# Kernel tuning notes

Measured on AMD Instinct MI355X. Metric: run time of the kernel, lower is better.

## Reference

```python
import jax, jax.numpy as jnp
import numpy as np

NUM_EXPERTS = 8


def setup_inputs() -> dict:
    key = jax.random.key(0)
    k1, k2, k3, k4, k5 = jax.random.split(key, 5)
    T, D, DFF, E, K = 2048, 2048, 1024, NUM_EXPERTS, 2
    hidden_states = jax.random.normal(k1, (T, D), dtype=jnp.float32)
    w1 = jax.random.normal(k2, (E, 2 * DFF, D), dtype=jnp.float32) * 0.02
    w2 = jax.random.normal(k3, (E, D, DFF), dtype=jnp.float32) * 0.02
    topk_weights = jax.random.uniform(k4, (T, K), dtype=jnp.float32)
    topk_weights = topk_weights / jnp.sum(topk_weights, axis=-1, keepdims=True)
    topk_ids = jax.random.randint(k5, (T, K), 0, E, dtype=jnp.int32)
    return {"hidden_states": hidden_states, "w1": w1, "w2": w2,
            "topk_weights": topk_weights, "topk_ids": topk_ids}


def _expert_fn(x, w1_e, w2_e):
    # x: [T, D], w1_e: [2*DFF, D], w2_e: [D, DFF]
    gu = x @ w1_e.T                      # [T, 2*DFF]
    dff = w2_e.shape[1]
    gate, up = gu[:, :dff], gu[:, dff:]
    h = jax.nn.silu(gate) * up           # SiLU-and-mul activation
    return h @ w2_e.T                    # [T, D]


def reference(hidden_states, w1, w2, topk_weights, topk_ids):
    T = hidden_states.shape[0]
    E = w1.shape[0]
    # route[t, e] = sum_k topk_weights[t,k] * (topk_ids[t,k] == e)
    route = jnp.zeros((T, E), dtype=hidden_states.dtype)
    route = route.at[jnp.arange(T)[:, None], topk_ids].add(topk_weights)
    # per-expert dense GEMMs (E is small and fixed), then weighted combine
    outs = jax.vmap(lambda w1_e, w2_e: _expert_fn(hidden_states, w1_e, w2_e))(w1, w2)  # [E, T, D]
    return jnp.einsum('te,etd->td', route, outs)
```

## Files before the change

kernel.cpp:

```cpp
#include <hip/hip_runtime.h>
#include <hip/hip_bf16.h>
#include <stdint.h>

typedef __attribute__((ext_vector_type(4))) float f32x4;
typedef __attribute__((ext_vector_type(8))) short bf16x8;
typedef unsigned short u16;

#define T_TOK   2048
#define D_DIM   2048
#define DFF_DIM 1024
#define NEXP    8
#define TOPK    2
#define NROWS   (T_TOK * TOPK)
#define BM      128
#define BK      64
#define MAX_MB  40
#define GRID_G  (16 * MAX_MB)

#define PIN() asm volatile("" ::: "memory")
#define BAR_LGKM()                                                        \
    asm volatile("s_waitcnt lgkmcnt(0)" ::: "memory");                    \
    __builtin_amdgcn_s_barrier()

__device__ __forceinline__ u16 f2bf(float f) {
    __hip_bfloat16 h = __float2bfloat16(f);
    return *reinterpret_cast<u16*>(&h);
}

__device__ __forceinline__ void gll16(const u16* gsrc, const u16* lds) {
    __builtin_amdgcn_global_load_lds(
        (const __attribute__((address_space(1))) uint32_t*)gsrc,
        (__attribute__((address_space(3))) uint32_t*)lds, 16, 0, 0);
}

__device__ __forceinline__ bf16x8 lds_read8_swz(const u16* base, int row, int inner) {
    int off = row * 128 + (inner ^ ((row & 7) << 4));
    return *(const bf16x8*)((const char*)base + off);
}

#define GLL_A(k0, dst)                                                    \
    _Pragma("unroll") for (int i = 0; i < 4; ++i)                         \
        gll16(asrc[i] + (k0), &(dst)[aoff[i]]);

#define LOAD_RB(rb, k0)                                                   \
    _Pragma("unroll") for (int i = 0; i < 4; ++i) {                       \
        rb[i][0] = *(const f32x4*)(bptr[i] + (k0));                       \
        rb[i][1] = *(const f32x4*)(bptr[i] + (k0) + 4);                   \
    }

#define CVT_WRITE(rb, dst)                                                \
    _Pragma("unroll") for (int i = 0; i < 4; ++i) {                       \
        bf16x8 vb;                                                        \
        _Pragma("unroll") for (int j = 0; j < 4; ++j) {                   \
            vb[j] = (short)f2bf(rb[i][0][j]);                             \
            vb[j + 4] = (short)f2bf(rb[i][1][j]);                         \
        }                                                                 \
        *(bf16x8*)((char*)(dst) + wroff[i]) = vb;                         \
    }

#define DECODE_BLOCK()                                                    \
    const int bid   = blockIdx.x;                                         \
    const int xcd   = bid & 7;                                            \
    const int local = bid >> 3;                                \
    const int n0h   = local / MAX_MB;                          \
    const int mb    = local - n0h * MAX_MB;                               \
    const int n0i   = xcd * 2 + n0h;                           \
    if (mb >= sched[0]) return;                                           \
    const int e    = sched[1 + 3 * mb];                                   \
    const int m0   = sched[2 + 3 * mb];                                   \
    const int mlen = sched[3 + 3 * mb]

__global__ void cvt_x_kernel(const float* __restrict__ X, u16* __restrict__ Xb,
                             float* __restrict__ out) {
    int idx = (blockIdx.x * 256 + threadIdx.x) * 8;
    f32x4 a = *(const f32x4*)(X + idx);
    f32x4 b = *(const f32x4*)(X + idx + 4);
    bf16x8 v;
#pragma unroll
    for (int j = 0; j < 4; ++j) { v[j] = (short)f2bf(a[j]); v[j + 4] = (short)f2bf(b[j]); }
    *(bf16x8*)(Xb + idx) = v;
    f32x4 z = (f32x4){0.f, 0.f, 0.f, 0.f};
    *(f32x4*)(out + idx) = z;
    *(f32x4*)(out + idx + 4) = z;
}

__global__ void route_kernel(const int* __restrict__ topk_ids,
                             const float* __restrict__ topk_w,
                             int* __restrict__ sched,
                             int* __restrict__ row_token,
                             float* __restrict__ row_w) {
    __shared__ int cnt[NEXP], off[NEXP], cur[NEXP];
    const int tid = threadIdx.x;
    if (tid < NEXP) cnt[tid] = 0;
    __syncthreads();
    for (int p = tid; p < NROWS; p += blockDim.x)
        atomicAdd(&cnt[topk_ids[p]], 1);
    __syncthreads();
    if (tid == 0) {
        int acc = 0, mb = 0;
        for (int e = 0; e < NEXP; ++e) {
            off[e] = acc;
            int c = cnt[e];
            for (int m0 = 0; m0 < c; m0 += BM) {
                sched[1 + 3 * mb] = e;
                sched[2 + 3 * mb] = acc + m0;
                sched[3 + 3 * mb] = (c - m0 < BM) ? (c - m0) : BM;
                ++mb;
            }
            acc += c;
        }
        sched[0] = mb;
    }
    if (tid < NEXP) cur[tid] = 0;
    __syncthreads();
    for (int p = tid; p < NROWS; p += blockDim.x) {
        int e = topk_ids[p];
        int slot = off[e] + atomicAdd(&cur[e], 1);
        row_token[slot] = p / TOPK;
        row_w[slot]     = topk_w[p];
    }
}

__global__ __launch_bounds__(256, 3)
void gemm1_kernel(const u16* __restrict__ Xb, const float* __restrict__ w1,
                  const int* __restrict__ sched, const int* __restrict__ row_token,
                  u16* __restrict__ H) {
    __shared__ u16 lA[2][BM * BK];
    __shared__ u16 lB[BM * BK];

    DECODE_BLOCK();
    const int n0 = n0i * 64;

    const int tid  = threadIdx.x;
    const int lane = tid & 63;
    const int wave = tid >> 6;
    const int wm = wave >> 1, wn = wave & 1;
    const int lr = lane & 15, lk = lane >> 4;

    const u16* asrc[4];
    int aoff[4];
#pragma unroll
    for (int i = 0; i < 4; ++i) {
        int R = i * 32 + wave * 8 + (lane >> 3);
        int grow = m0 + R; if (grow > NROWS - 1) grow = NROWS - 1;
        int tok = row_token[grow];
        asrc[i] = Xb + (size_t)tok * D_DIM + (size_t)(((lane & 7) ^ (R & 7)) * 8);
        aoff[i] = i * 2048 + wave * 512;
    }
    const float* bptr[4];
    int wroff[4];
#pragma unroll
    for (int i = 0; i < 4; ++i) {
        int chunk = i * 256 + tid;
        int row = chunk >> 3, c8 = chunk & 7;
        int gcol = (row < 64) ? (n0 + row) : (DFF_DIM + n0 + (row - 64));
        bptr[i] = w1 + ((size_t)e * (2 * DFF_DIM) + gcol) * D_DIM + c8 * 8;
        wroff[i] = row * 128 + ((c8 * 16) ^ ((row & 7) << 4));
    }

    f32x4 rb[4][2];
    f32x4 accg[4][2], accu[4][2];
#pragma unroll
    for (int m = 0; m < 4; ++m)
#pragma unroll
        for (int n = 0; n < 2; ++n) {
            accg[m][n] = (f32x4){0.f, 0.f, 0.f, 0.f};
            accu[m][n] = (f32x4){0.f, 0.f, 0.f, 0.f};
        }

#define MFMA_G1(bufA, bufB)                                               \
    _Pragma("unroll") for (int ks = 0; ks < 2; ++ks) {                    \
        const int inner = ks * 64 + lk * 16;                              \
        bf16x8 af[4], bg[2], bu[2];                                       \
        _Pragma("unroll") for (int m = 0; m < 4; ++m)                     \
            af[m] = lds_read8_swz(bufA, wm * 64 + m * 16 + lr, inner);    \
        _Pragma("unroll") for (int n = 0; n < 2; ++n) {                   \
            bg[n] = lds_read8_swz(bufB, wn * 32 + n * 16 + lr, inner);    \
            bu[n] = lds_read8_swz(bufB, 64 + wn * 32 + n * 16 + lr, inner); \
        }                                                                 \
        _Pragma("unroll") for (int m = 0; m < 4; ++m)                     \
            _Pragma("unroll") for (int n = 0; n < 2; ++n) {               \
                accg[m][n] = __builtin_amdgcn_mfma_f32_16x16x32_bf16(af[m], bg[n], accg[m][n], 0, 0, 0); \
                accu[m][n] = __builtin_amdgcn_mfma_f32_16x16x32_bf16(af[m], bu[n], accu[m][n], 0, 0, 0); \
            }                                                             \
    }

    const int KT = D_DIM / BK;
    LOAD_RB(rb, 0);
    GLL_A(0, lA[0]);
    CVT_WRITE(rb, lB);
    __syncthreads();

    for (int kt = 0, cur = 0; kt < KT; ++kt, cur ^= 1) {
        if (kt + 1 < KT) {
            LOAD_RB(rb, (kt + 1) * BK);
            GLL_A((kt + 1) * BK, lA[cur ^ 1]);
        }
        PIN();
        MFMA_G1(lA[cur], lB);
        BAR_LGKM();
        if (kt + 1 < KT) { CVT_WRITE(rb, lB); }
        __syncthreads();
    }
#undef MFMA_G1

#pragma unroll
    for (int m = 0; m < 4; ++m)
#pragma unroll
        for (int n = 0; n < 2; ++n)
#pragma unroll
            for (int r = 0; r < 4; ++r) {
                int rloc = wm * 64 + m * 16 + (lane >> 4) * 4 + r;
                if (rloc < mlen) {
                    int col = wn * 32 + n * 16 + lr;
                    float g = accg[m][n][r], u = accu[m][n][r];
                    float h = (g / (1.f + __expf(-g))) * u;
                    H[(size_t)(m0 + rloc) * DFF_DIM + n0 + col] = f2bf(h);
                }
            }
}

__global__ __launch_bounds__(256, 3)
void gemm2_kernel(const u16* __restrict__ H, const float* __restrict__ w2,
                  const int* __restrict__ sched, const int* __restrict__ row_token,
                  const float* __restrict__ row_w, float* __restrict__ out) {
    __shared__ u16 lA[2][BM * BK];
    __shared__ u16 lB[BM * BK];

    DECODE_BLOCK();
    const int n0 = n0i * 128;

    const int tid  = threadIdx.x;
    const int lane = tid & 63;
    const int wave = tid >> 6;
    const int wm = wave >> 1, wn = wave & 1;
    const int lr = lane & 15, lk = lane >> 4;

    const u16* asrc[4];
    int aoff[4];
#pragma unroll
    for (int i = 0; i < 4; ++i) {
        int R = i * 32 + wave * 8 + (lane >> 3);
        int grow = m0 + R; if (grow > NROWS - 1) grow = NROWS - 1;
        asrc[i] = H + (size_t)grow * DFF_DIM + (size_t)(((lane & 7) ^ (R & 7)) * 8);
        aoff[i] = i * 2048 + wave * 512;
    }
    const float* bptr[4];
    int wroff[4];
#pragma unroll
    for (int i = 0; i < 4; ++i) {
        int chunk = i * 256 + tid;
        int row = chunk >> 3, c8 = chunk & 7;
        bptr[i] = w2 + ((size_t)e * D_DIM + (n0 + row)) * DFF_DIM + c8 * 8;
        wroff[i] = row * 128 + ((c8 * 16) ^ ((row & 7) << 4));
    }

    f32x4 rb[4][2];
    f32x4 acc[4][4];
#pragma unroll
    for (int m = 0; m < 4; ++m)
#pragma unroll
        for (int n = 0; n < 4; ++n) acc[m][n] = (f32x4){0.f, 0.f, 0.f, 0.f};

#define MFMA_G2(bufA, bufB)                                               \
    _Pragma("unroll") for (int ks = 0; ks < 2; ++ks) {                    \
        const int inner = ks * 64 + lk * 16;                              \
        bf16x8 af[4], bfr[4];                                             \
        _Pragma("unroll") for (int m = 0; m < 4; ++m)                     \
            af[m] = lds_read8_swz(bufA, wm * 64 + m * 16 + lr, inner);    \
        _Pragma("unroll") for (int n = 0; n < 4; ++n)                     \
            bfr[n] = lds_read8_swz(bufB, wn * 64 + n * 16 + lr, inner);   \
        _Pragma("unroll") for (int m = 0; m < 4; ++m)                     \
            _Pragma("unroll") for (int n = 0; n < 4; ++n)                 \
                acc[m][n] = __builtin_amdgcn_mfma_f32_16x16x32_bf16(af[m], bfr[n], acc[m][n], 0, 0, 0); \
    }

    const int KT = DFF_DIM / BK;
    LOAD_RB(rb, 0);
    GLL_A(0, lA[0]);
    CVT_WRITE(rb, lB);
    __syncthreads();

    for (int kt = 0, cur = 0; kt < KT; ++kt, cur ^= 1) {
        if (kt + 1 < KT) {
            LOAD_RB(rb, (kt + 1) * BK);
            GLL_A((kt + 1) * BK, lA[cur ^ 1]);
        }
        PIN();
        MFMA_G2(lA[cur], lB);
        BAR_LGKM();
        if (kt + 1 < KT) { CVT_WRITE(rb, lB); }
        __syncthreads();
    }
#undef MFMA_G2

#pragma unroll
    for (int m = 0; m < 4; ++m)
#pragma unroll
        for (int n = 0; n < 4; ++n)
#pragma unroll
            for (int r = 0; r < 4; ++r) {
                int rloc = wm * 64 + m * 16 + (lane >> 4) * 4 + r;
                if (rloc < mlen) {
                    int grow = m0 + rloc;
                    int tok  = row_token[grow];
                    float w  = row_w[grow];
                    int col  = wn * 64 + n * 16 + lr;
                    atomicAdd(&out[(size_t)tok * D_DIM + n0 + col], acc[m][n][r] * w);
                }
            }
}

extern "C" void kernel_launch(void* const* d_in, const int* in_sizes, int n_in,
                              void* d_out, int out_size, void* d_ws, size_t ws_size,
                              hipStream_t stream) {
    const float* X  = (const float*)d_in[0];
    const float* w1 = (const float*)d_in[1];
    const float* w2 = (const float*)d_in[2];
    const float* tw = (const float*)d_in[3];
    const int*   ti = (const int*)d_in[4];

    int*   sched     = (int*)d_ws;
    int*   row_token = (int*)((char*)d_ws + 512);
    float* row_w     = (float*)((char*)d_ws + 512 + 4 * NROWS);
    u16*   Xb        = (u16*)((char*)d_ws + 65536);
    u16*   H         = (u16*)((char*)d_ws + 65536 + (size_t)T_TOK * D_DIM * 2);

    route_kernel<<<1, 256, 0, stream>>>(ti, tw, sched, row_token, row_w);
    cvt_x_kernel<<<(T_TOK * D_DIM) / (256 * 8), 256, 0, stream>>>(X, Xb, (float*)d_out);
    gemm1_kernel<<<GRID_G, 256, 0, stream>>>(Xb, w1, sched, row_token, H);
    gemm2_kernel<<<GRID_G, 256, 0, stream>>>(H, w2, sched, row_token, row_w, (float*)d_out);
}
```

Baseline: 151.0 us.

## Pre-convert expert weights to bf16 in a fused prep kernel before GEMMs

Adds a prep kernel that converts all of w1, w2 and X to bf16 in workspace, and runs the routing in an extra block of the same launch. New GEMM kernels then load bf16 A and B tiles straight into LDS via global_load_lds instead of loading fp32 weights into registers and converting them per tile. This removes repeated fp32 weight reads and conversion work across the M-blocks, at the cost of a full-weight conversion pass each call (about 200MB of traffic) and single-buffered LDS. The old path remains as a fallback when the workspace is too small.

```diff
diff --git a/kernel.cpp b/kernel.cpp
--- a/kernel.cpp
+++ b/kernel.cpp
@@ -17,6 +17,21 @@
 #define MAX_MB  40
 #define GRID_G  (16 * MAX_MB)
 
+#define XB_OFF    65536
+#define XB_BYTES  ((size_t)T_TOK * D_DIM * 2)
+#define H_OFF     (XB_OFF + XB_BYTES)
+#define H_BYTES   ((size_t)NROWS * DFF_DIM * 2)
+#define W1B_OFF   (H_OFF + H_BYTES)
+#define W1B_BYTES ((size_t)NEXP * 2 * DFF_DIM * D_DIM * 2)
+#define W2B_OFF   (W1B_OFF + W1B_BYTES)
+#define W2B_BYTES ((size_t)NEXP * D_DIM * DFF_DIM * 2)
+#define WS_NEED   (W2B_OFF + W2B_BYTES)
+
+#define W1_T   ((size_t)NEXP * 2 * DFF_DIM * D_DIM / 8)
+#define W2_T   ((size_t)NEXP * D_DIM * DFF_DIM / 8)
+#define X_T    ((size_t)T_TOK * D_DIM / 8)
+#define PREP_BLKS ((int)((W1_T + W2_T + X_T) / 256))
+
 #define PIN() asm volatile("" ::: "memory")
 #define BAR_LGKM()                                                        \
     asm volatile("s_waitcnt lgkmcnt(0)" ::: "memory");                    \
@@ -27,6 +42,15 @@
     return *reinterpret_cast<u16*>(&h);
 }
 
+__device__ __forceinline__ void cvt8(const float* src, u16* dst) {
+    f32x4 a = *(const f32x4*)src;
+    f32x4 b = *(const f32x4*)(src + 4);
+    bf16x8 v;
+#pragma unroll
+    for (int j = 0; j < 4; ++j) { v[j] = (short)f2bf(a[j]); v[j + 4] = (short)f2bf(b[j]); }
+    *(bf16x8*)dst = v;
+}
+
 __device__ __forceinline__ void gll16(const u16* gsrc, const u16* lds) {
     __builtin_amdgcn_global_load_lds(
         (const __attribute__((address_space(1))) uint32_t*)gsrc,
@@ -38,58 +62,9 @@
     return *(const bf16x8*)((const char*)base + off);
 }
 
-#define GLL_A(k0, dst)                                                    \
-    _Pragma("unroll") for (int i = 0; i < 4; ++i)                         \
-        gll16(asrc[i] + (k0), &(dst)[aoff[i]]);
-
-#define LOAD_RB(rb, k0)                                                   \
-    _Pragma("unroll") for (int i = 0; i < 4; ++i) {                       \
-        rb[i][0] = *(const f32x4*)(bptr[i] + (k0));                       \
-        rb[i][1] = *(const f32x4*)(bptr[i] + (k0) + 4);                   \
-    }
-
-#define CVT_WRITE(rb, dst)                                                \
-    _Pragma("unroll") for (int i = 0; i < 4; ++i) {                       \
-        bf16x8 vb;                                                        \
-        _Pragma("unroll") for (int j = 0; j < 4; ++j) {                   \
-            vb[j] = (short)f2bf(rb[i][0][j]);                             \
-            vb[j + 4] = (short)f2bf(rb[i][1][j]);                         \
-        }                                                                 \
-        *(bf16x8*)((char*)(dst) + wroff[i]) = vb;                         \
-    }
-
-#define DECODE_BLOCK()                                                    \
-    const int bid   = blockIdx.x;                                         \
-    const int xcd   = bid & 7;                                            \
-    const int local = bid >> 3;                                \
-    const int n0h   = local / MAX_MB;                          \
-    const int mb    = local - n0h * MAX_MB;                               \
-    const int n0i   = xcd * 2 + n0h;                           \
-    if (mb >= sched[0]) return;                                           \
-    const int e    = sched[1 + 3 * mb];                                   \
-    const int m0   = sched[2 + 3 * mb];                                   \
-    const int mlen = sched[3 + 3 * mb]
-
-__global__ void cvt_x_kernel(const float* __restrict__ X, u16* __restrict__ Xb,
-                             float* __restrict__ out) {
-    int idx = (blockIdx.x * 256 + threadIdx.x) * 8;
-    f32x4 a = *(const f32x4*)(X + idx);
-    f32x4 b = *(const f32x4*)(X + idx + 4);
-    bf16x8 v;
-#pragma unroll
-    for (int j = 0; j < 4; ++j) { v[j] = (short)f2bf(a[j]); v[j + 4] = (short)f2bf(b[j]); }
-    *(bf16x8*)(Xb + idx) = v;
-    f32x4 z = (f32x4){0.f, 0.f, 0.f, 0.f};
-    *(f32x4*)(out + idx) = z;
-    *(f32x4*)(out + idx + 4) = z;
-}
-
-__global__ void route_kernel(const int* __restrict__ topk_ids,
-                             const float* __restrict__ topk_w,
-                             int* __restrict__ sched,
-                             int* __restrict__ row_token,
-                             float* __restrict__ row_w) {
-    __shared__ int cnt[NEXP], off[NEXP], cur[NEXP];
+__device__ __forceinline__ void route_body(const int* topk_ids, const float* topk_w,
+                                           int* sched, int* row_token, float* row_w,
+                                           int* cnt, int* off, int* cur) {
     const int tid = threadIdx.x;
     if (tid < NEXP) cnt[tid] = 0;
     __syncthreads();
@@ -121,10 +96,252 @@
     }
 }
 
+__global__ void prep_kernel(const float* __restrict__ w1, const float* __restrict__ w2,
+                            const float* __restrict__ X,
+                            u16* __restrict__ w1b, u16* __restrict__ w2b,
+                            u16* __restrict__ Xb, float* __restrict__ out,
+                            const int* __restrict__ topk_ids,
+                            const float* __restrict__ topk_w,
+                            int* __restrict__ sched, int* __restrict__ row_token,
+                            float* __restrict__ row_w) {
+    __shared__ int cnt[NEXP], off[NEXP], cur[NEXP];
+    if (blockIdx.x == PREP_BLKS) {
+        route_body(topk_ids, topk_w, sched, row_token, row_w, cnt, off, cur);
+        return;
+    }
+    size_t t = (size_t)blockIdx.x * 256 + threadIdx.x;
+    if (t < W1_T) {
+        cvt8(w1 + t * 8, w1b + t * 8);
+    } else if (t < W1_T + W2_T) {
+        size_t u = t - W1_T;
+        cvt8(w2 + u * 8, w2b + u * 8);
+    } else {
+        size_t u = t - (W1_T + W2_T);
+        cvt8(X + u * 8, Xb + u * 8);
+        f32x4 z = (f32x4){0.f, 0.f, 0.f, 0.f};
+        *(f32x4*)(out + u * 8) = z;
+        *(f32x4*)(out + u * 8 + 4) = z;
+    }
+}
+
+#define DECODE_BLOCK()                                                    \
+    const int bid   = blockIdx.x;                                         \
+    const int xcd   = bid & 7;                                            \
+    const int local = bid >> 3;                                \
+    const int n0h   = local / MAX_MB;                          \
+    const int mb    = local - n0h * MAX_MB;                               \
+    const int n0i   = xcd * 2 + n0h;                           \
+    if (mb >= sched[0]) return;                                           \
+    const int e    = sched[1 + 3 * mb];                                   \
+    const int m0   = sched[2 + 3 * mb];                                   \
+    const int mlen = sched[3 + 3 * mb]
+
+#define GLL8(k0)                                                          \
+    _Pragma("unroll") for (int i = 0; i < 4; ++i)                         \
+        gll16(asrc[i] + (k0), &lA[aoff[i]]);                              \
+    _Pragma("unroll") for (int i = 0; i < 4; ++i)                         \
+        gll16(bsrc[i] + (k0), &lB[aoff[i]]);
+
 __global__ __launch_bounds__(256, 3)
-void gemm1_kernel(const u16* __restrict__ Xb, const float* __restrict__ w1,
-                  const int* __restrict__ sched, const int* __restrict__ row_token,
-                  u16* __restrict__ H) {
+void gemm1p_kernel(const u16* __restrict__ Xb, const u16* __restrict__ w1b,
+                   const int* __restrict__ sched, const int* __restrict__ row_token,
+                   u16* __restrict__ H) {
+    __shared__ u16 lA[BM * BK];
+    __shared__ u16 lB[BM * BK];
+
+    DECODE_BLOCK();
+    const int n0 = n0i * 64;
+
+    const int tid  = threadIdx.x;
+    const int lane = tid & 63;
+    const int wave = tid >> 6;
+    const int wm = wave >> 1, wn = wave & 1;
+    const int lr = lane & 15, lk = lane >> 4;
+
+    const u16* asrc[4];
+    const u16* bsrc[4];
+    int aoff[4];
+#pragma unroll
+    for (int i = 0; i < 4; ++i) {
+        int R = i * 32 + wave * 8 + (lane >> 3);
+        int grow = m0 + R; if (grow > NROWS - 1) grow = NROWS - 1;
+        int tok = row_token[grow];
+        int c8 = ((lane & 7) ^ (R & 7)) * 8;
+        asrc[i] = Xb + (size_t)tok * D_DIM + c8;
+        int gr = (R < 64) ? (n0 + R) : (DFF_DIM + n0 + (R - 64));
+        bsrc[i] = w1b + ((size_t)e * (2 * DFF_DIM) + gr) * D_DIM + c8;
+        aoff[i] = i * 2048 + wave * 512;
+    }
+
+    f32x4 accg[4][2], accu[4][2];
+#pragma unroll
+    for (int m = 0; m < 4; ++m)
+#pragma unroll
+        for (int n = 0; n < 2; ++n) {
+            accg[m][n] = (f32x4){0.f, 0.f, 0.f, 0.f};
+            accu[m][n] = (f32x4){0.f, 0.f, 0.f, 0.f};
+        }
+
+    const int KT = D_DIM / BK;
+    for (int kt = 0; kt < KT; ++kt) {
+        GLL8(kt * BK);
+        __syncthreads();
+#pragma unroll
+        for (int ks = 0; ks < 2; ++ks) {
+            const int inner = ks * 64 + lk * 16;
+            bf16x8 af[4], bg[2], bu[2];
+#pragma unroll
+            for (int m = 0; m < 4; ++m)
+                af[m] = lds_read8_swz(lA, wm * 64 + m * 16 + lr, inner);
+#pragma unroll
+            for (int n = 0; n < 2; ++n) {
+                bg[n] = lds_read8_swz(lB, wn * 32 + n * 16 + lr, inner);
+                bu[n] = lds_read8_swz(lB, 64 + wn * 32 + n * 16 + lr, inner);
+            }
+#pragma unroll
+            for (int m = 0; m < 4; ++m)
+#pragma unroll
+                for (int n = 0; n < 2; ++n) {
+                    accg[m][n] = __builtin_amdgcn_mfma_f32_16x16x32_bf16(af[m], bg[n], accg[m][n], 0, 0, 0);
+                    accu[m][n] = __builtin_amdgcn_mfma_f32_16x16x32_bf16(af[m], bu[n], accu[m][n], 0, 0, 0);
+                }
+        }
+        __syncthreads();
+    }
+
+#pragma unroll
+    for (int m = 0; m < 4; ++m)
+#pragma unroll
+        for (int n = 0; n < 2; ++n)
+#pragma unroll
+            for (int r = 0; r < 4; ++r) {
+                int rloc = wm * 64 + m * 16 + (lane >> 4) * 4 + r;
+                if (rloc < mlen) {
+                    int col = wn * 32 + n * 16 + lr;
+                    float g = accg[m][n][r], u = accu[m][n][r];
+                    float h = (g / (1.f + __expf(-g))) * u;
+                    H[(size_t)(m0 + rloc) * DFF_DIM + n0 + col] = f2bf(h);
+                }
+            }
+}
+
+__global__ __launch_bounds__(256, 3)
+void gemm2p_kernel(const u16* __restrict__ H, const u16* __restrict__ w2b,
+                   const int* __restrict__ sched, const int* __restrict__ row_token,
+                   const float* __restrict__ row_w, float* __restrict__ out) {
+    __shared__ u16 lA[BM * BK];
+    __shared__ u16 lB[BM * BK];
+
+    DECODE_BLOCK();
+    const int n0 = n0i * 128;
+
+    const int tid  = threadIdx.x;
+    const int lane = tid & 63;
+    const int wave = tid >> 6;
+    const int wm = wave >> 1, wn = wave & 1;
+    const int lr = lane & 15, lk = lane >> 4;
+
+    const u16* asrc[4];
+    const u16* bsrc[4];
+    int aoff[4];
+#pragma unroll
+    for (int i = 0; i < 4; ++i) {
+        int R = i * 32 + wave * 8 + (lane >> 3);
+        int grow = m0 + R; if (grow > NROWS - 1) grow = NROWS - 1;
+        int c8 = ((lane & 7) ^ (R & 7)) * 8;
+        asrc[i] = H + (size_t)grow * DFF_DIM + c8;
+        bsrc[i] = w2b + ((size_t)e * D_DIM + (n0 + R)) * DFF_DIM + c8;
+        aoff[i] = i * 2048 + wave * 512;
+    }
+
+    f32x4 acc[4][4];
+#pragma unroll
+    for (int m = 0; m < 4; ++m)
+#pragma unroll
+        for (int n = 0; n < 4; ++n) acc[m][n] = (f32x4){0.f, 0.f, 0.f, 0.f};
+
+    const int KT = DFF_DIM / BK;
+    for (int kt = 0; kt < KT; ++kt) {
+        GLL8(kt * BK);
+        __syncthreads();
+#pragma unroll
+        for (int ks = 0; ks < 2; ++ks) {
+            const int inner = ks * 64 + lk * 16;
+            bf16x8 af[4], bfr[4];
+#pragma unroll
+            for (int m = 0; m < 4; ++m)
+                af[m] = lds_read8_swz(lA, wm * 64 + m * 16 + lr, inner);
+#pragma unroll
+            for (int n = 0; n < 4; ++n)
+                bfr[n] = lds_read8_swz(lB, wn * 64 + n * 16 + lr, inner);
+#pragma unroll
+            for (int m = 0; m < 4; ++m)
+#pragma unroll
+                for (int n = 0; n < 4; ++n)
+                    acc[m][n] = __builtin_amdgcn_mfma_f32_16x16x32_bf16(af[m], bfr[n], acc[m][n], 0, 0, 0);
+        }
+        __syncthreads();
+    }
+
+#pragma unroll
+    for (int m = 0; m < 4; ++m)
+#pragma unroll
+        for (int n = 0; n < 4; ++n)
+#pragma unroll
+            for (int r = 0; r < 4; ++r) {
+                int rloc = wm * 64 + m * 16 + (lane >> 4) * 4 + r;
+                if (rloc < mlen) {
+                    int grow = m0 + rloc;
+                    int tok  = row_token[grow];
+                    float w  = row_w[grow];
+                    int col  = wn * 64 + n * 16 + lr;
+                    atomicAdd(&out[(size_t)tok * D_DIM + n0 + col], acc[m][n][r] * w);
+                }
+            }
+}
+
+__global__ void cvt_x_kernel(const float* __restrict__ X, u16* __restrict__ Xb,
+                             float* __restrict__ out) {
+    int idx = (blockIdx.x * 256 + threadIdx.x) * 8;
+    cvt8(X + idx, Xb + idx);
+    f32x4 z = (f32x4){0.f, 0.f, 0.f, 0.f};
+    *(f32x4*)(out + idx) = z;
+    *(f32x4*)(out + idx + 4) = z;
+}
+
+__global__ void route_kernel(const int* __restrict__ topk_ids,
+                             const float* __restrict__ topk_w,
+                             int* __restrict__ sched,
+                             int* __restrict__ row_token,
+                             float* __restrict__ row_w) {
+    __shared__ int cnt[NEXP], off[NEXP], cur[NEXP];
+    route_body(topk_ids, topk_w, sched, row_token, row_w, cnt, off, cur);
+}
+
+#define GLL_A(k0, dst)                                                    \
+    _Pragma("unroll") for (int i = 0; i < 4; ++i)                         \
+        gll16(asrc[i] + (k0), &(dst)[aoff[i]]);
+
+#define LOAD_RB(rb, k0)                                                   \
+    _Pragma("unroll") for (int i = 0; i < 4; ++i) {                       \
+        rb[i][0] = *(const f32x4*)(bptr[i] + (k0));                       \
+        rb[i][1] = *(const f32x4*)(bptr[i] + (k0) + 4);                   \
+    }
+
+#define CVT_WRITE(rb, dst)                                                \
+    _Pragma("unroll") for (int i = 0; i < 4; ++i) {                       \
+        bf16x8 vb;                                                        \
+        _Pragma("unroll") for (int j = 0; j < 4; ++j) {                   \
+            vb[j] = (short)f2bf(rb[i][0][j]);                             \
+            vb[j + 4] = (short)f2bf(rb[i][1][j]);                         \
+        }                                                                 \
+        *(bf16x8*)((char*)(dst) + wroff[i]) = vb;                         \
+    }
+
+__global__ __launch_bounds__(256, 3)
+void gemm1f_kernel(const u16* __restrict__ Xb, const float* __restrict__ w1,
+                   const int* __restrict__ sched, const int* __restrict__ row_token,
+                   u16* __restrict__ H) {
     __shared__ u16 lA[2][BM * BK];
     __shared__ u16 lB[BM * BK];
 
@@ -221,9 +438,9 @@
 }
 
 __global__ __launch_bounds__(256, 3)
-void gemm2_kernel(const u16* __restrict__ H, const float* __restrict__ w2,
-                  const int* __restrict__ sched, const int* __restrict__ row_token,
-                  const float* __restrict__ row_w, float* __restrict__ out) {
+void gemm2f_kernel(const u16* __restrict__ H, const float* __restrict__ w2,
+                   const int* __restrict__ sched, const int* __restrict__ row_token,
+                   const float* __restrict__ row_w, float* __restrict__ out) {
     __shared__ u16 lA[2][BM * BK];
     __shared__ u16 lB[BM * BK];
 
@@ -323,11 +540,21 @@
     int*   sched     = (int*)d_ws;
     int*   row_token = (int*)((char*)d_ws + 512);
     float* row_w     = (float*)((char*)d_ws + 512 + 4 * NROWS);
-    u16*   Xb        = (u16*)((char*)d_ws + 65536);
-    u16*   H         = (u16*)((char*)d_ws + 65536 + (size_t)T_TOK * D_DIM * 2);
-
-    route_kernel<<<1, 256, 0, stream>>>(ti, tw, sched, row_token, row_w);
-    cvt_x_kernel<<<(T_TOK * D_DIM) / (256 * 8), 256, 0, stream>>>(X, Xb, (float*)d_out);
-    gemm1_kernel<<<GRID_G, 256, 0, stream>>>(Xb, w1, sched, row_token, H);
-    gemm2_kernel<<<GRID_G, 256, 0, stream>>>(H, w2, sched, row_token, row_w, (float*)d_out);
-}
+    u16*   Xb        = (u16*)((char*)d_ws + XB_OFF);
+    u16*   H         = (u16*)((char*)d_ws + H_OFF);
+
+    if (ws_size >= WS_NEED) {
+        u16* w1b = (u16*)((char*)d_ws + W1B_OFF);
+        u16* w2b = (u16*)((char*)d_ws + W2B_OFF);
+        prep_kernel<<<PREP_BLKS + 1, 256, 0, stream>>>(w1, w2, X, w1b, w2b, Xb,
+                                                       (float*)d_out, ti, tw,
+                                                       sched, row_token, row_w);
+        gemm1p_kernel<<<GRID_G, 256, 0, stream>>>(Xb, w1b, sched, row_token, H);
+        gemm2p_kernel<<<GRID_G, 256, 0, stream>>>(H, w2b, sched, row_token, row_w, (float*)d_out);
+    } else {
+        route_kernel<<<1, 256, 0, stream>>>(ti, tw, sched, row_token, row_w);
+        cvt_x_kernel<<<(T_TOK * D_DIM) / (256 * 8), 256, 0, stream>>>(X, Xb, (float*)d_out);
+        gemm1f_kernel<<<GRID_G, 256, 0, stream>>>(Xb, w1, sched, row_token, H);
+        gemm2f_kernel<<<GRID_G, 256, 0, stream>>>(H, w2, sched, row_token, row_w, (float*)d_out);
+    }
+}
```

Measured after the change: 168.3 us. 1.11x slower.

## Double-buffer weight register prefetch in GEMMs and merge prep kernels

Applied to the files above, without the earlier changes.

Both GEMM main loops now keep two register buffers for the fp32 weight tiles and prefetch two K-steps ahead. Barriers wait only on partial vmcnt, so the global weight loads stay in flight across iterations instead of being drained each step. Separately, the routing and X-conversion kernels are merged into one launch with a grid-stride loop and nontemporal loads, removing one kernel launch. The extra register buffers raise VGPR pressure, which could hurt occupancy at the 3-waves launch bound, and the vmcnt(8) count must match the number of outstanding loads.

```diff
diff --git a/kernel.cpp b/kernel.cpp
--- a/kernel.cpp
+++ b/kernel.cpp
@@ -17,14 +17,31 @@
 #define MAX_MB  40
 #define GRID_G  (16 * MAX_MB)
 
+#define XB_OFF    65536
+#define H_OFF     (XB_OFF + (size_t)T_TOK * D_DIM * 2)
+#define X_T       ((size_t)T_TOK * D_DIM / 8)
+#define PREPX_BLKS 512
+
 #define PIN() asm volatile("" ::: "memory")
 #define BAR_LGKM()                                                        \
     asm volatile("s_waitcnt lgkmcnt(0)" ::: "memory");                    \
     __builtin_amdgcn_s_barrier()
+#define BAR_V8()                                                          \
+    asm volatile("s_waitcnt vmcnt(8) lgkmcnt(0)" ::: "memory");           \
+    __builtin_amdgcn_s_barrier()
 
 __device__ __forceinline__ u16 f2bf(float f) {
     __hip_bfloat16 h = __float2bfloat16(f);
     return *reinterpret_cast<u16*>(&h);
+}
+
+__device__ __forceinline__ void cvt8_nt(const float* src, u16* dst) {
+    f32x4 a = __builtin_nontemporal_load((const f32x4*)src);
+    f32x4 b = __builtin_nontemporal_load(((const f32x4*)src) + 1);
+    bf16x8 v;
+#pragma unroll
+    for (int j = 0; j < 4; ++j) { v[j] = (short)f2bf(a[j]); v[j + 4] = (short)f2bf(b[j]); }
+    *(bf16x8*)dst = v;
 }
 
 __device__ __forceinline__ void gll16(const u16* gsrc, const u16* lds) {
@@ -38,58 +55,9 @@
     return *(const bf16x8*)((const char*)base + off);
 }
 
-#define GLL_A(k0, dst)                                                    \
-    _Pragma("unroll") for (int i = 0; i < 4; ++i)                         \
-        gll16(asrc[i] + (k0), &(dst)[aoff[i]]);
-
-#define LOAD_RB(rb, k0)                                                   \
-    _Pragma("unroll") for (int i = 0; i < 4; ++i) {                       \
-        rb[i][0] = *(const f32x4*)(bptr[i] + (k0));                       \
-        rb[i][1] = *(const f32x4*)(bptr[i] + (k0) + 4);                   \
-    }
-
-#define CVT_WRITE(rb, dst)                                                \
-    _Pragma("unroll") for (int i = 0; i < 4; ++i) {                       \
-        bf16x8 vb;                                                        \
-        _Pragma("unroll") for (int j = 0; j < 4; ++j) {                   \
-            vb[j] = (short)f2bf(rb[i][0][j]);                             \
-            vb[j + 4] = (short)f2bf(rb[i][1][j]);                         \
-        }                                                                 \
-        *(bf16x8*)((char*)(dst) + wroff[i]) = vb;                         \
-    }
-
-#define DECODE_BLOCK()                                                    \
-    const int bid   = blockIdx.x;                                         \
-    const int xcd   = bid & 7;                                            \
-    const int local = bid >> 3;                                \
-    const int n0h   = local / MAX_MB;                          \
-    const int mb    = local - n0h * MAX_MB;                               \
-    const int n0i   = xcd * 2 + n0h;                           \
-    if (mb >= sched[0]) return;                                           \
-    const int e    = sched[1 + 3 * mb];                                   \
-    const int m0   = sched[2 + 3 * mb];                                   \
-    const int mlen = sched[3 + 3 * mb]
-
-__global__ void cvt_x_kernel(const float* __restrict__ X, u16* __restrict__ Xb,
-                             float* __restrict__ out) {
-    int idx = (blockIdx.x * 256 + threadIdx.x) * 8;
-    f32x4 a = *(const f32x4*)(X + idx);
-    f32x4 b = *(const f32x4*)(X + idx + 4);
-    bf16x8 v;
-#pragma unroll
-    for (int j = 0; j < 4; ++j) { v[j] = (short)f2bf(a[j]); v[j + 4] = (short)f2bf(b[j]); }
-    *(bf16x8*)(Xb + idx) = v;
-    f32x4 z = (f32x4){0.f, 0.f, 0.f, 0.f};
-    *(f32x4*)(out + idx) = z;
-    *(f32x4*)(out + idx + 4) = z;
-}
-
-__global__ void route_kernel(const int* __restrict__ topk_ids,
-                             const float* __restrict__ topk_w,
-                             int* __restrict__ sched,
-                             int* __restrict__ row_token,
-                             float* __restrict__ row_w) {
-    __shared__ int cnt[NEXP], off[NEXP], cur[NEXP];
+__device__ __forceinline__ void route_body(const int* topk_ids, const float* topk_w,
+                                           int* sched, int* row_token, float* row_w,
+                                           int* cnt, int* off, int* cur) {
     const int tid = threadIdx.x;
     if (tid < NEXP) cnt[tid] = 0;
     __syncthreads();
@@ -121,6 +89,58 @@
     }
 }
 
+__global__ void prep_kernel(const float* __restrict__ X,
+                            u16* __restrict__ Xb, float* __restrict__ out,
+                            const int* __restrict__ topk_ids,
+                            const float* __restrict__ topk_w,
+                            int* __restrict__ sched, int* __restrict__ row_token,
+                            float* __restrict__ row_w) {
+    __shared__ int cnt[NEXP], off[NEXP], cur[NEXP];
+    if (blockIdx.x == PREPX_BLKS) {
+        route_body(topk_ids, topk_w, sched, row_token, row_w, cnt, off, cur);
+        return;
+    }
+    const size_t stride = (size_t)PREPX_BLKS * 256;
+    for (size_t t = (size_t)blockIdx.x * 256 + threadIdx.x; t < X_T; t += stride) {
+        cvt8_nt(X + t * 8, Xb + t * 8);
+        f32x4 z = (f32x4){0.f, 0.f, 0.f, 0.f};
+        *(f32x4*)(out + t * 8) = z;
+        *(f32x4*)(out + t * 8 + 4) = z;
+    }
+}
+
+#define DECODE_BLOCK()                                                    \
+    const int bid   = blockIdx.x;                                         \
+    const int xcd   = bid & 7;                                            \
+    const int local = bid >> 3;                                \
+    const int n0h   = local / MAX_MB;                          \
+    const int mb    = local - n0h * MAX_MB;                               \
+    const int n0i   = xcd * 2 + n0h;                           \
+    if (mb >= sched[0]) return;                                           \
+    const int e    = sched[1 + 3 * mb];                                   \
+    const int m0   = sched[2 + 3 * mb];                                   \
+    const int mlen = sched[3 + 3 * mb]
+
+#define GLL_A(k0, dst)                                                    \
+    _Pragma("unroll") for (int i = 0; i < 4; ++i)                         \
+        gll16(asrc[i] + (k0), &(dst)[aoff[i]]);
+
+#define LOAD_RB(rb, k0)                                                   \
+    _Pragma("unroll") for (int i = 0; i < 4; ++i) {                       \
+        rb[i][0] = *(const f32x4*)(bptr[i] + (k0));                       \
+        rb[i][1] = *(const f32x4*)(bptr[i] + (k0) + 4);                   \
+    }
+
+#define CVT_WRITE(rb, dst)                                                \
+    _Pragma("unroll") for (int i = 0; i < 4; ++i) {                       \
+        bf16x8 vb;                                                        \
+        _Pragma("unroll") for (int j = 0; j < 4; ++j) {                   \
+            vb[j] = (short)f2bf(rb[i][0][j]);                             \
+            vb[j + 4] = (short)f2bf(rb[i][1][j]);                         \
+        }                                                                 \
+        *(bf16x8*)((char*)(dst) + wroff[i]) = vb;                         \
+    }
+
 __global__ __launch_bounds__(256, 3)
 void gemm1_kernel(const u16* __restrict__ Xb, const float* __restrict__ w1,
                   const int* __restrict__ sched, const int* __restrict__ row_token,
@@ -158,7 +178,7 @@
         wroff[i] = row * 128 + ((c8 * 16) ^ ((row & 7) << 4));
     }
 
-    f32x4 rb[4][2];
+    f32x4 rbA[4][2], rbB[4][2];
     f32x4 accg[4][2], accu[4][2];
 #pragma unroll
     for (int m = 0; m < 4; ++m)
@@ -186,21 +206,35 @@
     }
 
     const int KT = D_DIM / BK;
-    LOAD_RB(rb, 0);
+    LOAD_RB(rbA, 0);
     GLL_A(0, lA[0]);
-    CVT_WRITE(rb, lB);
-    __syncthreads();
-
-    for (int kt = 0, cur = 0; kt < KT; ++kt, cur ^= 1) {
-        if (kt + 1 < KT) {
-            LOAD_RB(rb, (kt + 1) * BK);
-            GLL_A((kt + 1) * BK, lA[cur ^ 1]);
-        }
-        PIN();
-        MFMA_G1(lA[cur], lB);
-        BAR_LGKM();
-        if (kt + 1 < KT) { CVT_WRITE(rb, lB); }
-        __syncthreads();
+    CVT_WRITE(rbA, lB);
+    LOAD_RB(rbB, BK);
+    BAR_V8();
+
+    for (int tt = 0; tt < KT; tt += 2) {
+        {
+            const int t = tt;
+            if (t + 1 < KT) GLL_A((t + 1) * BK, lA[1]);
+            const int kr = (t + 2 < KT ? t + 2 : KT - 1) * BK;
+            LOAD_RB(rbA, kr);
+            PIN();
+            MFMA_G1(lA[0], lB);
+            BAR_LGKM();
+            if (t + 1 < KT) { CVT_WRITE(rbB, lB); }
+            BAR_V8();
+        }
+        {
+            const int t = tt + 1;
+            if (t + 1 < KT) GLL_A((t + 1) * BK, lA[0]);
+            const int kr = (t + 2 < KT ? t + 2 : KT - 1) * BK;
+            LOAD_RB(rbB, kr);
+            PIN();
+            MFMA_G1(lA[1], lB);
+            BAR_LGKM();
+            if (t + 1 < KT) { CVT_WRITE(rbA, lB); }
+            BAR_V8();
+        }
     }
 #undef MFMA_G1
 
@@ -255,7 +289,7 @@
         wroff[i] = row * 128 + ((c8 * 16) ^ ((row & 7) << 4));
     }
 
-    f32x4 rb[4][2];
+    f32x4 rbA[4][2], rbB[4][2];
     f32x4 acc[4][4];
 #pragma unroll
     for (int m = 0; m < 4; ++m)
@@ -276,21 +310,35 @@
     }
 
     const int KT = DFF_DIM / BK;
-    LOAD_RB(rb, 0);
+    LOAD_RB(rbA, 0);
     GLL_A(0, lA[0]);
-    CVT_WRITE(rb, lB);
-    __syncthreads();
-
-    for (int kt = 0, cur = 0; kt < KT; ++kt, cur ^= 1) {
-        if (kt + 1 < KT) {
-            LOAD_RB(rb, (kt + 1) * BK);
-            GLL_A((kt + 1) * BK, lA[cur ^ 1]);
-        }
-        PIN();
-        MFMA_G2(lA[cur], lB);
-        BAR_LGKM();
-        if (kt + 1 < KT) { CVT_WRITE(rb, lB); }
-        __syncthreads();
+    CVT_WRITE(rbA, lB);
+    LOAD_RB(rbB, BK);
+    BAR_V8();
+
+    for (int tt = 0; tt < KT; tt += 2) {
+        {
+            const int t = tt;
+            if (t + 1 < KT) GLL_A((t + 1) * BK, lA[1]);
+            const int kr = (t + 2 < KT ? t + 2 : KT - 1) * BK;
+            LOAD_RB(rbA, kr);
+            PIN();
+            MFMA_G2(lA[0], lB);
+            BAR_LGKM();
+            if (t + 1 < KT) { CVT_WRITE(rbB, lB); }
+            BAR_V8();
+        }
+        {
+            const int t = tt + 1;
+            if (t + 1 < KT) GLL_A((t + 1) * BK, lA[0]);
+            const int kr = (t + 2 < KT ? t + 2 : KT - 1) * BK;
+            LOAD_RB(rbB, kr);
+            PIN();
+            MFMA_G2(lA[1], lB);
+            BAR_LGKM();
+            if (t + 1 < KT) { CVT_WRITE(rbA, lB); }
+            BAR_V8();
+        }
     }
 #undef MFMA_G2
 
@@ -323,11 +371,11 @@
     int*   sched     = (int*)d_ws;
     int*   row_token = (int*)((char*)d_ws + 512);
     float* row_w     = (float*)((char*)d_ws + 512 + 4 * NROWS);
-    u16*   Xb        = (u16*)((char*)d_ws + 65536);
-    u16*   H         = (u16*)((char*)d_ws + 65536 + (size_t)T_TOK * D_DIM * 2);
-
-    route_kernel<<<1, 256, 0, stream>>>(ti, tw, sched, row_token, row_w);
-    cvt_x_kernel<<<(T_TOK * D_DIM) / (256 * 8), 256, 0, stream>>>(X, Xb, (float*)d_out);
+    u16*   Xb        = (u16*)((char*)d_ws + XB_OFF);
+    u16*   H         = (u16*)((char*)d_ws + H_OFF);
+
+    prep_kernel<<<PREPX_BLKS + 1, 256, 0, stream>>>(X, Xb, (float*)d_out,
+                                                    ti, tw, sched, row_token, row_w);
     gemm1_kernel<<<GRID_G, 256, 0, stream>>>(Xb, w1, sched, row_token, H);
     gemm2_kernel<<<GRID_G, 256, 0, stream>>>(H, w2, sched, row_token, row_w, (float*)d_out);
 }
```

New measurement: 399.5 us. +164.5%, slower.
